# Optimization experiments

Hardware: AMD Instinct MI355X
Metric: run time of the kernel (lower is better)

Reference implementation:

```python
import jax, jax.numpy as jnp
from jax import lax
import numpy as np
import math

A = 9          # anchors per location
NC = 80        # classes
SCORE_T = 0.05
NMS_T = 0.5
DPI = 100      # detections_per_img (also per-level K in _inference)
BBOX_CLIP = math.log(1000.0 / 16.0)
LEVEL_SHAPES = [(64, 64), (32, 32), (16, 16), (8, 8)]
STRIDES = [8, 16, 32, 64]
BASE_SIZES = [32, 64, 128, 256]


def _conv(x, w, b):
    y = lax.conv_general_dilated(x, w, (1, 1), 'SAME', dimension_numbers=('NCHW', 'OIHW', 'NCHW'))
    return y + b[None, :, None, None]


def _head(feats, tower_w, tower_b, out_w, out_b, out_dim):
    outs = []
    for f in feats:
        x = f
        for i in range(tower_w.shape[0]):
            x = jax.nn.relu(_conv(x, tower_w[i], tower_b[i]))
        x = _conv(x, out_w, out_b)                     # [B, A*out_dim, H, W]
        B, _, H, W = x.shape
        x = x.reshape(B, A, out_dim, H, W).transpose(0, 3, 4, 1, 2).reshape(B, H * W * A, out_dim)
        outs.append(x)
    return outs


def _clip_boxes(b, img_h, img_w):
    x1 = jnp.clip(b[:, 0], 0.0, float(img_w)); y1 = jnp.clip(b[:, 1], 0.0, float(img_h))
    x2 = jnp.clip(b[:, 2], 0.0, float(img_w)); y2 = jnp.clip(b[:, 3], 0.0, float(img_h))
    return jnp.stack([x1, y1, x2, y2], axis=-1)


def _level_anchors(H, W, stride, s, img_h, img_w):
    # torchvision AnchorGenerator: sizes (s, s*2^(1/3), s*2^(2/3)), ratios (0.5,1,2)
    sizes = jnp.array([s, int(s * 2 ** (1 / 3)), int(s * 2 ** (2 / 3))], dtype=jnp.float32)
    ratios = jnp.array([0.5, 1.0, 2.0], dtype=jnp.float32)
    h_r = jnp.sqrt(ratios); w_r = 1.0 / h_r
    ws = (w_r[:, None] * sizes[None, :]).reshape(-1)
    hs = (h_r[:, None] * sizes[None, :]).reshape(-1)
    base = jnp.round(jnp.stack([-ws, -hs, ws, hs], axis=-1) / 2.0)   # [9,4]
    sx = (jnp.arange(W) * stride).astype(jnp.float32)
    sy = (jnp.arange(H) * stride).astype(jnp.float32)
    yy, xx = jnp.meshgrid(sy, sx, indexing='ij')
    shifts = jnp.stack([xx, yy, xx, yy], axis=-1).reshape(-1, 1, 4)   # [H*W,1,4]
    anch = (shifts + base[None]).reshape(-1, 4)                        # [H*W*A,4]
    return _clip_boxes(anch, img_h, img_w)


def _decode(rel, anch):
    # BoxCoder.decode_single with weights (1,1,1,1)
    w = anch[:, 2] - anch[:, 0]; h = anch[:, 3] - anch[:, 1]
    cx = anch[:, 0] + 0.5 * w;   cy = anch[:, 1] + 0.5 * h
    dx, dy = rel[:, 0], rel[:, 1]
    dw = jnp.minimum(rel[:, 2], BBOX_CLIP)
    dh = jnp.minimum(rel[:, 3], BBOX_CLIP)
    pcx = dx * w + cx; pcy = dy * h + cy
    pw = jnp.exp(dw) * w; ph = jnp.exp(dh) * h
    return jnp.stack([pcx - 0.5 * pw, pcy - 0.5 * ph, pcx + 0.5 * pw, pcy + 0.5 * ph], axis=-1)


def _pairwise_iou(boxes):
    area = (boxes[:, 2] - boxes[:, 0]) * (boxes[:, 3] - boxes[:, 1])
    lt = jnp.maximum(boxes[:, None, :2], boxes[None, :, :2])
    rb = jnp.minimum(boxes[:, None, 2:], boxes[None, :, 2:])
    wh = jnp.clip(rb - lt, 0.0)
    inter = wh[..., 0] * wh[..., 1]
    return inter / (area[:, None] + area[None, :] - inter + 1e-9)


def _per_image(logits, regs, anchors, img_h, img_w):
    bs, ss, ls = [], [], []
    for logit, reg, anch in zip(logits, regs, anchors):
        scores = jax.nn.sigmoid(logit).reshape(-1)                   # [N*NC]
        masked = jnp.where(scores > SCORE_T, scores, -1.0)
        top_s, idx = lax.top_k(masked, DPI)                          # fixed K = detections_per_img
        aidx = idx // NC
        lbl = idx % NC
        boxes = _clip_boxes(_decode(reg[aidx], anch[aidx]), img_h, img_w)
        valid = top_s > SCORE_T
        bs.append(boxes)
        ss.append(jnp.where(valid, top_s, -1.0))
        ls.append(jnp.where(valid, lbl, -1))
    boxes = jnp.concatenate(bs, 0); scores = jnp.concatenate(ss, 0); labels = jnp.concatenate(ls, 0)
    # batched (per-class) NMS via label coordinate offsets
    order = jnp.argsort(-scores)
    boxes_s = boxes[order]; scores_s = scores[order]; labels_s = labels[order]
    offset = labels_s.astype(boxes.dtype) * (float(max(img_h, img_w)) + 1.0)
    iou = lax.stop_gradient(_pairwise_iou(boxes_s + offset[:, None]))
    N = scores_s.shape[0]
    ar = jnp.arange(N)
    def body(i, keep):
        sup = keep[i] & (iou[i] > NMS_T) & (ar > i)
        return keep & ~sup
    keep = lax.fori_loop(0, N, body, scores_s > SCORE_T)
    fs, fi = lax.top_k(jnp.where(keep, scores_s, -1.0), DPI)
    ok = fs > SCORE_T
    fb = jnp.where(ok[:, None], boxes_s[fi], 0.0)
    fl = jnp.where(ok, labels_s[fi], -1)
    fs = jnp.where(ok, fs, 0.0)
    return fb, fs, fl


def setup_inputs() -> dict:
    key = jax.random.key(0)
    ks = jax.random.split(key, 8)
    B = 4
    w_scale = 0.04
    inp = {}
    shapes = [(B, 256, 64, 64), (B, 256, 32, 32), (B, 256, 16, 16), (B, 256, 8, 8)]
    for i, sh in enumerate(shapes):
        inp[f'f{i}'] = jax.random.normal(ks[i], sh, dtype=jnp.float32)
    inp['cls_tower_w'] = jax.random.normal(ks[4], (4, 256, 256, 3, 3), dtype=jnp.float32) * w_scale
    inp['cls_tower_b'] = jnp.zeros((4, 256), dtype=jnp.float32)
    inp['cls_out_w'] = jax.random.normal(ks[5], (A * NC, 256, 3, 3), dtype=jnp.float32) * w_scale
    inp['cls_out_b'] = jnp.full((A * NC,), -2.0, dtype=jnp.float32)  # prior-like bias
    inp['reg_tower_w'] = jax.random.normal(ks[6], (4, 256, 256, 3, 3), dtype=jnp.float32) * w_scale
    inp['reg_tower_b'] = jnp.zeros((4, 256), dtype=jnp.float32)
    inp['reg_out_w'] = jax.random.normal(ks[7], (A * 4, 256, 3, 3), dtype=jnp.float32) * w_scale
    inp['reg_out_b'] = jnp.zeros((A * 4,), dtype=jnp.float32)
    inp['image_h'] = 512
    inp['image_w'] = 512
    return inp


def reference(f0, f1, f2, f3, cls_tower_w, cls_tower_b, cls_out_w, cls_out_b,
              reg_tower_w, reg_tower_b, reg_out_w, reg_out_b, image_h, image_w):
    feats = [f0, f1, f2, f3]
    cls_logits = _head(feats, cls_tower_w, cls_tower_b, cls_out_w, cls_out_b, NC)   # list of [B,Ni,NC]
    bbox_regs = _head(feats, reg_tower_w, reg_tower_b, reg_out_w, reg_out_b, 4)     # list of [B,Ni,4]
    anchors = [_level_anchors(H, W, st, s, image_h, image_w)
               for (H, W), st, s in zip(LEVEL_SHAPES, STRIDES, BASE_SIZES)]
    fn = lambda ls, rs: _per_image(ls, rs, anchors, image_h, image_w)
    boxes, scores, labels = jax.vmap(fn)(tuple(cls_logits), tuple(bbox_regs))
    return boxes, scores, labels
```

## Files before the change

### kernel.cpp

```cpp
#include <hip/hip_runtime.h>
#include <math.h>

#define A_NUM 9
#define NCLS 80
#define IMG_KEY 3916800
#define IMG_REG 195840
#define CAP 8192
#define HBINS 16384

#define PCHUNK 12032
#define CHUNK_SLOTS 24064
#define CHUNK_BYTES (CHUNK_SLOTS * 16)
#define ACT_SLAB ((size_t)CHUNK_BYTES * 16)
#define WCHUNK_BYTES 40960
#define WCOG_BYTES (WCHUNK_BYTES * 16)

typedef _Float16 h8 __attribute__((ext_vector_type(8)));
typedef float fx4 __attribute__((ext_vector_type(4)));
typedef unsigned short u16;

__constant__ int   c_W[4]       = {64, 32, 16, 8};
__constant__ int   c_stride[4]  = {8, 16, 32, 64};
__constant__ float c_sizes[4][3]= {{32.f,40.f,50.f},{64.f,80.f,101.f},{128.f,161.f,203.f},{256.f,322.f,406.f}};
__constant__ int   c_keyOff[4]  = {0, 2949120, 3686400, 3870720};
__constant__ int   c_keyCnt[4]  = {2949120, 737280, 184320, 46080};
__constant__ int   c_regOff[4]  = {0, 147456, 184320, 193536};
__constant__ int   c_C[4]       = {66, 34, 18, 18};
__constant__ int   c_plvl[4]    = {0, 8712, 11024, 11672};
__constant__ int   c_pOff[4]    = {0, 1024, 1280, 1344};

__device__ __forceinline__ void gl_lds16(const void* g, void* l) {
    __builtin_amdgcn_global_load_lds(
        (const __attribute__((address_space(1))) void*)g,
        (__attribute__((address_space(3))) void*)l, 16, 0, 0);
}

__global__ __launch_bounds__(256) void pad16_k(
    const float* __restrict__ f0, const float* __restrict__ f1,
    const float* __restrict__ f2, const float* __restrict__ f3,
    char* __restrict__ Pin)
{
    int idx = blockIdx.x * 256 + threadIdx.x;
    const int PER_IMG = 16 * 2 * 1360;
    if (idx >= 4 * PER_IMG) return;
    int img = idx / PER_IMG;
    int r = idx - img * PER_IMG;
    int chunk = r / (2 * 1360);
    int r2 = r - chunk * (2 * 1360);
    int hfsel = r2 / 1360;
    int p = r2 - hfsel * 1360;
    int lvl = (p < 1024) ? 0 : (p < 1280 ? 1 : (p < 1344 ? 2 : 3));
    int u = p - c_pOff[lvl];
    int sh = 4 - lvl;
    int y = u >> sh;
    int xg = u & ((1 << sh) - 1);
    int x0 = xg * 4;
    int W = 64 >> lvl;
    const float* f = (lvl == 0) ? f0 : (lvl == 1) ? f1 : (lvl == 2) ? f2 : f3;
    int ci0 = chunk * 16 + hfsel * 8;
    float4 v[8];
    #pragma unroll
    for (int j = 0; j < 8; ++j)
        v[j] = *reinterpret_cast<const float4*>(
            f + ((size_t)(img * 256 + ci0 + j)) * (W * W) + y * W + x0);
    char* base = Pin + (size_t)img * ACT_SLAB + (size_t)chunk * CHUNK_BYTES;
    const int C = c_C[lvl];
    size_t rowSlot = (size_t)c_plvl[lvl] + (size_t)((y + 1) * 2 + hfsel) * C;
    #pragma unroll
    for (int c = 0; c < 4; ++c) {
        h8 hv, lv;
        #pragma unroll
        for (int j = 0; j < 8; ++j) {
            float val = (c == 0) ? v[j].x : (c == 1) ? v[j].y : (c == 2) ? v[j].z : v[j].w;
            _Float16 hh = (_Float16)val;
            hv[j] = hh;
            lv[j] = (_Float16)(val - (float)hh);
        }
        size_t slot = rowSlot + (x0 + c + 1);
        *reinterpret_cast<h8*>(base + slot * 16) = hv;
        *reinterpret_cast<h8*>(base + (slot + PCHUNK) * 16) = lv;
    }
}

__global__ __launch_bounds__(256) void repack16_k(
    const float* __restrict__ src, u16* __restrict__ dst,
    int C_out, int nCg, int total)
{
    int idx = blockIdx.x * 256 + threadIdx.x;
    if (idx >= total) return;
    int per = nCg * 16 * 1280;
    int layer = idx / per;
    int r = idx - layer * per;
    int cg = r / (16 * 1280);
    int r2 = r - cg * (16 * 1280);
    int chunk = r2 / 1280;
    int s = r2 - chunk * 1280;
    int co = s & 63;
    int r3 = s >> 6;
    int hfsel = r3 & 1;
    int kk = r3 >> 1;
    int coG = cg * 64 + co;
    float v[8];
    if (kk < 9 && coG < C_out) {
        const float* sp = src + ((size_t)(layer * C_out + coG)) * 2304
                        + (size_t)(chunk * 16 + hfsel * 8) * 9 + kk;
        #pragma unroll
        for (int j = 0; j < 8; ++j) v[j] = sp[j * 9];
    } else {
        #pragma unroll
        for (int j = 0; j < 8; ++j) v[j] = 0.f;
    }
    h8 hv, lv;
    #pragma unroll
    for (int j = 0; j < 8; ++j) {
        _Float16 hh = (_Float16)v[j];
        hv[j] = hh;
        lv[j] = (_Float16)(v[j] - (float)hh);
    }
    size_t e = ((size_t)((layer * nCg + cg) * 16 + chunk)) * 20480
             + (size_t)(kk >> 1) * 2048 + (size_t)(kk & 1) * 1024
             + (size_t)hfsel * 512 + (size_t)co * 8;
    *reinterpret_cast<h8*>(dst + e) = hv;
    *reinterpret_cast<h8*>(dst + e + 10240) = lv;
}

__global__ __launch_bounds__(256, 3) void conv16(
    const char* __restrict__ Pin, const char* __restrict__ bufIn, char* __restrict__ bufOut,
    const u16* __restrict__ repA, const float* __restrict__ bA,
    const u16* __restrict__ repB, const float* __restrict__ bB,
    unsigned* __restrict__ keys, float* __restrict__ regb,
    int mode, int usePin)
{
    const int tid = threadIdx.x;
    const int lane = tid & 63;
    const int wv = tid >> 6;

    int img, head, coBase, C_out, epi, tile;
    if (mode == 0) {
        int hw = blockIdx.x;
        int logical = (hw & 7) * 88 + (hw >> 3);
        int z = logical / 88;
        int rem = logical - z * 88;
        tile = rem >> 2;
        coBase = (rem & 3) * 64;
        img = z & 3; head = z >> 2;
        C_out = 256; epi = 0;
    } else {
        int hw = blockIdx.x;
        int logical = (hw & 7) * 143 + (hw >> 3);
        img = logical / 286;
        int rem = logical - img * 286;
        tile = rem / 13;
        int yy = rem - tile * 13;
        if (yy < 12) { head = 0; coBase = yy * 64; C_out = 720; epi = 1; }
        else         { head = 1; coBase = 0;       C_out = 36;  epi = 2; }
    }
    const float* bsel = head ? bB : bA;
    const u16* wsel = head ? repB : repA;
    const char* wBase = (const char*)wsel + (size_t)(coBase >> 6) * WCOG_BYTES;

    int lvl, ty, tx;
    if (tile < 16)      { lvl = 0; ty = tile >> 2; tx = tile & 3; }
    else if (tile < 20) { int u = tile - 16; lvl = 1; ty = u >> 1; tx = u & 1; }
    else if (tile == 20){ lvl = 2; ty = 0; tx = 0; }
    else                { lvl = 3; ty = 0; tx = 0; }
    const int W = 64 >> lvl;
    const int C = c_C[lvl];
    const int plvl = c_plvl[lvl];
    const int tileY = ty * 16, tileX = tx * 16;

    const char* srcB = usePin ? Pin + (size_t)img * ACT_SLAB
                              : bufIn + (size_t)(head * 4 + img) * ACT_SLAB;

    __shared__ alignas(16) char sA[10368];
    __shared__ alignas(16) char sB[20480];

    const int laneCol = lane & 15;
    const int g = lane >> 4;
    const int halfS = g & 1;
    const int tapS = g >> 1;
    const int laneBv = tapS * 2048 + halfS * 1024 + laneCol * 16;
    int laneAhi[5];
    int AloOff[5];
    #pragma unroll
    for (int k = 0; k < 5; ++k) {
        int kk = 2 * k + tapS; if (kk > 8) kk = 8;
        int ky = kk / 3;
        int kx = kk - ky * 3;
        laneAhi[k] = ky * 576 + halfS * 288 + (laneCol + kx) * 16;
        AloOff[k] = PCHUNK * 16
                  + (plvl + ((tileY + wv * 4 + ky) * 2 + halfS) * C
                     + tileX + laneCol + kx) * 16;
    }
    const int mtStride = 2 * C * 16;

    int aByte[3]; bool aOk[3];
    #pragma unroll
    for (int p = 0; p < 3; ++p) {
        int s = tid + 256 * p;
        aOk[p] = (s < 648);
        int sc = aOk[p] ? s : 647;
        int row = sc / 36;
        int q = sc - row * 36;
        int hf = q / 18;
        int col = q - hf * 18;
        aByte[p] = (plvl + ((tileY + row) * 2 + hf) * C + tileX + col) * 16;
    }

    fx4 acc[4][4];
    #pragma unroll
    for (int mt = 0; mt < 4; ++mt)
        #pragma unroll
        for (int nt = 0; nt < 4; ++nt)
            acc[mt][nt] = (fx4){0.f, 0.f, 0.f, 0.f};

    #pragma unroll 1
    for (int ck = 0; ck < 16; ++ck) {
        const char* srcCk = srcB + (size_t)ck * CHUNK_BYTES;
        const char* wCk = wBase + (size_t)ck * WCHUNK_BYTES;
        const char* wLo = wCk + 20480;

        h8 Bl[2][4];
        #pragma unroll
        for (int nt = 0; nt < 4; ++nt)
            Bl[0][nt] = *reinterpret_cast<const h8*>(wLo + laneBv + nt * 256);

        #pragma unroll
        for (int p = 0; p < 3; ++p)
            if (aOk[p]) gl_lds16(srcCk + aByte[p], (char*)sA + (wv * 64 + 256 * p) * 16);
        for (int j = wv; j < 20; j += 4)
            gl_lds16(wCk + j * 1024 + lane * 16, (char*)sB + j * 1024);
        __syncthreads();

        #pragma unroll
        for (int k = 0; k < 5; ++k) {
            if (k < 4) {
                const char* wn = wLo + (k + 1) * 4096;
                #pragma unroll
                for (int nt = 0; nt < 4; ++nt)
                    Bl[(k + 1) & 1][nt] = *reinterpret_cast<const h8*>(wn + laneBv + nt * 256);
            }
            h8 Al[4];
            #pragma unroll
            for (int mt = 0; mt < 4; ++mt)
                Al[mt] = *reinterpret_cast<const h8*>(srcCk + AloOff[k] + mt * mtStride);
            const char* bk = sB + k * 4096;
            h8 Bh[4];
            #pragma unroll
            for (int nt = 0; nt < 4; ++nt)
                Bh[nt] = *reinterpret_cast<const h8*>(bk + laneBv + nt * 256);
            #pragma unroll
            for (int mt = 0; mt < 4; ++mt) {
                h8 Ah = *reinterpret_cast<const h8*>(sA + (wv * 4 + mt) * 576 + laneAhi[k]);
                #pragma unroll
                for (int nt = 0; nt < 4; ++nt) {
                    acc[mt][nt] = __builtin_amdgcn_mfma_f32_16x16x32_f16(Ah, Bh[nt], acc[mt][nt], 0, 0, 0);
                    acc[mt][nt] = __builtin_amdgcn_mfma_f32_16x16x32_f16(Ah, Bl[k & 1][nt], acc[mt][nt], 0, 0, 0);
                    acc[mt][nt] = __builtin_amdgcn_mfma_f32_16x16x32_f16(Al[mt], Bh[nt], acc[mt][nt], 0, 0, 0);
                }
            }
        }
        __syncthreads();
    }

    const int HW = W * W;
    if (epi == 0) {
        char* dstB = bufOut + (size_t)(head * 4 + img) * ACT_SLAB;
        _Float16* eW = reinterpret_cast<_Float16*>(sB + wv * 1024);
        const int ci8 = laneCol & 7;
        const int hf  = laneCol >> 3;
        const int rpx = lane & 15, rhalf = (lane >> 4) & 1, rplane = lane >> 5;
        const int rOff = rpx * 32 + rplane * 16 + rhalf * 8;
        const int rx = tileX + rpx;
        #pragma unroll
        for (int mt = 0; mt < 4; ++mt) {
            int y = tileY + wv * 4 + mt;
            bool yok = (y < W);
            #pragma unroll
            for (int nt = 0; nt < 4; ++nt) {
                int coG = coBase + nt * 16 + laneCol;
                float b = bsel[coG];
                #pragma unroll
                for (int i = 0; i < 4; ++i) {
                    float v = fmaxf(acc[mt][nt][i] + b, 0.f);
                    _Float16 hh = (_Float16)v;
                    _Float16 ll = (_Float16)(v - (float)hh);
                    int px = g * 4 + i;
                    eW[px * 32 + hf * 8 + ci8] = hh;
                    eW[px * 32 + 16 + hf * 8 + ci8] = ll;
                }
                __syncthreads();
                if (yok && rx < W) {
                    int chunkIdx = (coBase + nt * 16) >> 4;
                    size_t slot = (size_t)chunkIdx * CHUNK_SLOTS + (size_t)rplane * PCHUNK
                                + plvl + (size_t)((y + 1) * 2 + rhalf) * C + (rx + 1);
                    *reinterpret_cast<h8*>(dstB + slot * 16) =
                        *reinterpret_cast<const h8*>(eW + rOff);
                }
                __syncthreads();
            }
        }
    } else if (epi == 1) {
        unsigned* kb = keys + (size_t)img * IMG_KEY + c_keyOff[lvl];
        #pragma unroll
        for (int mt = 0; mt < 4; ++mt) {
            int y = tileY + wv * 4 + mt;
            int x0 = tileX + g * 4;
            if (y >= W || x0 >= W) continue;
            #pragma unroll
            for (int nt = 0; nt < 4; ++nt) {
                int coG = coBase + nt * 16 + laneCol;
                if (coG >= C_out) continue;
                float b = bsel[coG];
                unsigned kq[4];
                #pragma unroll
                for (int i = 0; i < 4; ++i) {
                    float sc = 1.0f / (1.0f + expf(-(acc[mt][nt][i] + b)));
                    kq[i] = (sc > 0.05f) ? __float_as_uint(sc) : 0u;
                }
                *reinterpret_cast<uint4*>(kb + (size_t)coG * HW + y * W + x0) =
                    make_uint4(kq[0], kq[1], kq[2], kq[3]);
            }
        }
    } else {
        float* rb = regb + (size_t)img * IMG_REG + c_regOff[lvl];
        #pragma unroll
        for (int mt = 0; mt < 4; ++mt) {
            int y = tileY + wv * 4 + mt;
            if (y >= W) continue;
            #pragma unroll
            for (int nt = 0; nt < 4; ++nt) {
                int coG = nt * 16 + laneCol;
                if (coG >= C_out) continue;
                float b = bsel[coG];
                int a = coG >> 2, jj = coG & 3;
                #pragma unroll
                for (int i = 0; i < 4; ++i) {
                    int x = tileX + g * 4 + i;
                    if (x >= W) continue;
                    rb[((size_t)(y * W + x) * A_NUM + a) * 4 + jj] = acc[mt][nt][i] + b;
                }
            }
        }
    }
}

__global__ __launch_bounds__(256) void hist_k(const unsigned* __restrict__ keys,
                                              unsigned* __restrict__ hist)
{
    int il = blockIdx.y, img = il >> 2, lvl = il & 3;
    int n = c_keyCnt[lvl];
    int chunk = blockIdx.x * 16384;
    if (chunk >= n) return;
    __shared__ unsigned h[HBINS];
    for (int t = threadIdx.x; t < HBINS; t += 256) h[t] = 0;
    __syncthreads();
    const uint4* k4 = (const uint4*)(keys + (size_t)img * IMG_KEY + c_keyOff[lvl]);
    int i0 = chunk >> 2, i1 = min(chunk + 16384, n) >> 2;
    for (int i = i0 + (int)threadIdx.x; i < i1; i += 256) {
        uint4 kv = k4[i];
        if (kv.x) atomicAdd(&h[kv.x >> 18], 1u);
        if (kv.y) atomicAdd(&h[kv.y >> 18], 1u);
        if (kv.z) atomicAdd(&h[kv.z >> 18], 1u);
        if (kv.w) atomicAdd(&h[kv.w >> 18], 1u);
    }
    __syncthreads();
    unsigned* gh = hist + (size_t)il * HBINS;
    for (int t = threadIdx.x; t < HBINS; t += 256)
        if (h[t]) atomicAdd(&gh[t], h[t]);
}

__global__ __launch_bounds__(256) void thresh_k(const unsigned* __restrict__ hist,
                                                unsigned* __restrict__ tbin)
{
    const unsigned* h = hist + (size_t)blockIdx.x * HBINS;
    __shared__ unsigned cs[256];
    int tid = threadIdx.x;
    unsigned s = 0;
    int base = tid * 64;
    for (int q = 0; q < 64; ++q) { int b = base + q; if (b >= 1) s += h[b]; }
    cs[tid] = s;
    __syncthreads();
    if (tid == 0) {
        unsigned total = 0, sel = 0;
        for (int c = 255; c >= 0; --c) {
            if (total + cs[c] >= 100u) {
                int lo = (c == 0) ? 1 : c * 64;
                for (int b = c * 64 + 63; b >= lo; --b) {
                    total += h[b];
                    if (total >= 100u) { sel = (unsigned)b; break; }
                }
                break;
            }
            total += cs[c];
        }
        tbin[blockIdx.x] = sel;
    }
}

__global__ __launch_bounds__(256) void compact_k(const unsigned* __restrict__ keys,
                                                 const unsigned* __restrict__ tbin,
                                                 unsigned* __restrict__ cnt,
                                                 uint2* __restrict__ comp)
{
    int il = blockIdx.y, img = il >> 2, lvl = il & 3;
    int n = c_keyCnt[lvl];
    int chunk = blockIdx.x * 16384;
    if (chunk >= n) return;
    const uint4* k4 = (const uint4*)(keys + (size_t)img * IMG_KEY + c_keyOff[lvl]);
    unsigned thr = tbin[il] << 18;
    int shift = 12 - 2 * lvl;
    int hwm = (1 << shift) - 1;
    int i0 = chunk >> 2, i1 = min(chunk + 16384, n) >> 2;
    __shared__ unsigned lcnt, lbase, lcur;
    if (threadIdx.x == 0) { lcnt = 0; lcur = 0; }
    __syncthreads();
    unsigned myc = 0;
    for (int i = i0 + (int)threadIdx.x; i < i1; i += 256) {
        uint4 kv = k4[i];
        myc += (kv.x != 0u && kv.x >= thr);
        myc += (kv.y != 0u && kv.y >= thr);
        myc += (kv.z != 0u && kv.z >= thr);
        myc += (kv.w != 0u && kv.w >= thr);
    }
    if (myc) atomicAdd(&lcnt, myc);
    __syncthreads();
    if (threadIdx.x == 0 && lcnt) lbase = atomicAdd(&cnt[il], lcnt);
    __syncthreads();
    if (lcnt == 0) return;
    uint2* c = comp + (size_t)il * CAP;
    for (int i = i0 + (int)threadIdx.x; i < i1; i += 256) {
        uint4 kv = k4[i];
        unsigned kk[4] = {kv.x, kv.y, kv.z, kv.w};
        #pragma unroll
        for (int j = 0; j < 4; ++j) {
            unsigned key = kk[j];
            if (key != 0u && key >= thr) {
                int t = i * 4 + j;
                int co = t >> shift, p = t & hwm;
                int a = co / NCLS, cls = co - a * NCLS;
                unsigned idx = (unsigned)((p * A_NUM + a) * NCLS + cls);
                unsigned pos = lbase + atomicAdd(&lcur, 1u);
                if (pos < CAP) c[pos] = make_uint2(key, idx);
            }
        }
    }
}

__global__ __launch_bounds__(256) void topsort_k(const unsigned* __restrict__ cnt,
                                                 const uint2* __restrict__ comp,
                                                 uint2* __restrict__ topk)
{
    __shared__ unsigned long long s[CAP];
    int il = blockIdx.x, tid = threadIdx.x;
    int n = (int)min(cnt[il], (unsigned)CAP);
    const uint2* c = comp + (size_t)il * CAP;
    for (int i = tid; i < CAP; i += 256) {
        unsigned long long v = 0ull;
        if (i < n) {
            uint2 e = c[i];
            v = ((unsigned long long)e.x << 32) | (unsigned long long)(~e.y);
        }
        s[i] = v;
    }
    for (int k = 2; k <= CAP; k <<= 1) {
        for (int j = k >> 1; j > 0; j >>= 1) {
            __syncthreads();
            for (int p = tid; p < CAP / 2; p += 256) {
                int i = ((p & ~(j - 1)) << 1) | (p & (j - 1));
                int ixj = i | j;
                unsigned long long a = s[i], b = s[ixj];
                if (((i & k) == 0) ? (a < b) : (a > b)) { s[i] = b; s[ixj] = a; }
            }
        }
    }
    __syncthreads();
    if (tid < 100) {
        unsigned long long v = s[tid];
        topk[il * 100 + tid] = make_uint2((unsigned)(v >> 32), ~(unsigned)(v & 0xFFFFFFFFull));
    }
}

__global__ void decode_k(const uint2* __restrict__ topk, const float* __restrict__ regb,
                         float* __restrict__ cboxes, float* __restrict__ cscores,
                         int* __restrict__ clabels, const int* __restrict__ ph, const int* __restrict__ pw)
{
    int il = blockIdx.x, img = il >> 2, lvl = il & 3;
    int j = threadIdx.x;
    if (j >= 100) return;
    float imgW = (float)pw[0], imgH = (float)ph[0];
    uint2 tk = topk[il * 100 + j];
    int outP = img * 400 + lvl * 100 + j;
    if (tk.x == 0u) {
        cboxes[outP * 4 + 0] = 0.f; cboxes[outP * 4 + 1] = 0.f;
        cboxes[outP * 4 + 2] = 0.f; cboxes[outP * 4 + 3] = 0.f;
        cscores[outP] = -1.0f; clabels[outP] = -1;
        return;
    }
    float score = __uint_as_float(tk.x);
    unsigned idx = tk.y;
    int aidx = (int)(idx / NCLS);
    int lbl  = (int)(idx - (unsigned)aidx * NCLS);
    int a = aidx % A_NUM, p = aidx / A_NUM;
    int W = c_W[lvl];
    int y = p / W, x = p - y * W;
    int r = a / 3, si = a - r * 3;
    float ratio = (r == 0) ? 0.5f : ((r == 1) ? 1.0f : 2.0f);
    float size = c_sizes[lvl][si];
    float hr = sqrtf(ratio);
    float wr = 1.0f / hr;
    float wsz = wr * size, hsz = hr * size;
    float bw = rintf(wsz * 0.5f), bh = rintf(hsz * 0.5f);
    float sx = (float)(x * c_stride[lvl]), sy = (float)(y * c_stride[lvl]);
    float ax1 = fminf(fmaxf(sx - bw, 0.f), imgW);
    float ay1 = fminf(fmaxf(sy - bh, 0.f), imgH);
    float ax2 = fminf(fmaxf(sx + bw, 0.f), imgW);
    float ay2 = fminf(fmaxf(sy + bh, 0.f), imgH);
    float aw = ax2 - ax1, ah = ay2 - ay1;
    float cx = ax1 + 0.5f * aw, cy = ay1 + 0.5f * ah;
    const float* rel = regb + (size_t)img * IMG_REG + c_regOff[lvl] + (size_t)aidx * 4;
    float dx = rel[0], dy = rel[1];
    float dw = fminf(rel[2], 4.135166556742356f);
    float dh = fminf(rel[3], 4.135166556742356f);
    float pcx = dx * aw + cx, pcy = dy * ah + cy;
    float pwd = expf(dw) * aw, phd = expf(dh) * ah;
    float x1 = pcx - 0.5f * pwd, y1 = pcy - 0.5f * phd;
    float x2 = pcx + 0.5f * pwd, y2 = pcy + 0.5f * phd;
    cboxes[outP * 4 + 0] = fminf(fmaxf(x1, 0.f), imgW);
    cboxes[outP * 4 + 1] = fminf(fmaxf(y1, 0.f), imgH);
    cboxes[outP * 4 + 2] = fminf(fmaxf(x2, 0.f), imgW);
    cboxes[outP * 4 + 3] = fminf(fmaxf(y2, 0.f), imgH);
    cscores[outP] = score;
    clabels[outP] = lbl;
}

__global__ __launch_bounds__(512) void nms_k(const float* __restrict__ cboxes,
                                             const float* __restrict__ cscores,
                                             const int* __restrict__ clabels,
                                             const int* __restrict__ ph, const int* __restrict__ pw,
                                             float* __restrict__ out)
{
    int img = blockIdx.x, tid = threadIdx.x;
    __shared__ float sSc[512];
    __shared__ int   sPos[512];
    __shared__ float bx1[400], by1[400], bx2[400], by2[400], sAr[400];
    __shared__ int   sKeep[400], sLbl[400];
    float imgH = (float)ph[0], imgW = (float)pw[0];
    float offm = fmaxf(imgH, imgW) + 1.0f;

    sSc[tid] = (tid < 400) ? cscores[img * 400 + tid] : -3.0f;
    sPos[tid] = tid;
    __syncthreads();

    for (int k = 2; k <= 512; k <<= 1) {
        for (int jj = k >> 1; jj > 0; jj >>= 1) {
            int ixj = tid ^ jj;
            if (ixj > tid) {
                float s1 = sSc[tid], s2 = sSc[ixj];
                int p1 = sPos[tid], p2 = sPos[ixj];
                bool bef = (s1 > s2) || (s1 == s2 && p1 < p2);
                bool sw = ((tid & k) == 0) ? (!bef) : bef;
                if (sw) { sSc[tid] = s2; sSc[ixj] = s1; sPos[tid] = p2; sPos[ixj] = p1; }
            }
            __syncthreads();
        }
    }

    if (tid < 400) {
        int p = sPos[tid];
        int lbl = clabels[img * 400 + p];
        float ofs = (float)lbl * offm;
        float x1 = cboxes[(img * 400 + p) * 4 + 0] + ofs;
        float y1 = cboxes[(img * 400 + p) * 4 + 1] + ofs;
        float x2 = cboxes[(img * 400 + p) * 4 + 2] + ofs;
        float y2 = cboxes[(img * 400 + p) * 4 + 3] + ofs;
        bx1[tid] = x1; by1[tid] = y1; bx2[tid] = x2; by2[tid] = y2;
        sAr[tid] = (x2 - x1) * (y2 - y1);
        sLbl[tid] = lbl;
        sKeep[tid] = (sSc[tid] > 0.05f) ? 1 : 0;
    }
    __syncthreads();

    for (int i = 0; i < 400; ++i) {
        if (sKeep[i]) {
            for (int j2 = i + 1 + tid; j2 < 400; j2 += 512) {
                float ltx = fmaxf(bx1[i], bx1[j2]), lty = fmaxf(by1[i], by1[j2]);
                float rbx = fminf(bx2[i], bx2[j2]), rby = fminf(by2[i], by2[j2]);
                float ww = fmaxf(rbx - ltx, 0.f), hh = fmaxf(rby - lty, 0.f);
                float inter = ww * hh;
                float iou = inter / (((sAr[i] + sAr[j2]) - inter) + 1e-9f);
                if (iou > 0.5f) sKeep[j2] = 0;
            }
        }
        __syncthreads();
    }

    if (tid == 0) {
        int rank = 0;
        for (int i = 0; i < 400 && rank < 100; ++i) {
            if (sKeep[i]) {
                int p = sPos[i];
                for (int kk = 0; kk < 4; ++kk)
                    out[(img * 100 + rank) * 4 + kk] = cboxes[(img * 400 + p) * 4 + kk];
                out[1600 + img * 100 + rank] = sSc[i];
                out[2000 + img * 100 + rank] = (float)sLbl[i];
                ++rank;
            }
        }
        for (; rank < 100; ++rank) {
            for (int kk = 0; kk < 4; ++kk) out[(img * 100 + rank) * 4 + kk] = 0.f;
            out[1600 + img * 100 + rank] = 0.f;
            out[2000 + img * 100 + rank] = -1.0f;
        }
    }
}

extern "C" void kernel_launch(void* const* d_in, const int* in_sizes, int n_in,
                              void* d_out, int out_size, void* d_ws, size_t ws_size,
                              hipStream_t stream)
{
    const float* f0 = (const float*)d_in[0];
    const float* f1 = (const float*)d_in[1];
    const float* f2 = (const float*)d_in[2];
    const float* f3 = (const float*)d_in[3];
    const float* cls_tw = (const float*)d_in[4];
    const float* cls_tb = (const float*)d_in[5];
    const float* cls_ow = (const float*)d_in[6];
    const float* cls_ob = (const float*)d_in[7];
    const float* reg_tw = (const float*)d_in[8];
    const float* reg_tb = (const float*)d_in[9];
    const float* reg_ow = (const float*)d_in[10];
    const float* reg_ob = (const float*)d_in[11];
    const int* ph = (const int*)d_in[12];
    const int* pw = (const int*)d_in[13];
    float* out = (float*)d_out;

    char* ws = (char*)d_ws;
    size_t off = 0;
    auto alloc = [&](size_t bytes) -> void* {
        void* p = ws + off;
        off = (off + bytes + 1023) & ~(size_t)1023;
        return p;
    };
    const size_t KEYS = (size_t)4 * IMG_KEY * 4;
    const size_t ACT8 = ACT_SLAB * 8;
    char*     Pin    = (char*)alloc(ACT_SLAB * 4 + 32768);
    char*     slabA  = (char*)alloc((KEYS > ACT8 ? KEYS : ACT8) + 32768);
    unsigned* keys   = (unsigned*)slabA;
    char*     actA   = slabA;
    char*     actB   = (char*)alloc(ACT8 + 32768);
    u16*      repCT  = (u16*)alloc((size_t)16 * WCOG_BYTES);
    u16*      repRT  = (u16*)alloc((size_t)16 * WCOG_BYTES);
    u16*      repCO  = (u16*)alloc((size_t)12 * WCOG_BYTES);
    u16*      repRO  = (u16*)alloc((size_t)1 * WCOG_BYTES);
    float*    regb   = (float*)alloc((size_t)4 * IMG_REG * 4);
    unsigned* hist   = (unsigned*)alloc((size_t)16 * HBINS * 4);
    unsigned* cnt    = (unsigned*)alloc(16 * 4);
    unsigned* tbin   = (unsigned*)alloc(16 * 4);
    uint2*    comp   = (uint2*)alloc((size_t)16 * CAP * 8);
    uint2*    topk   = (uint2*)alloc((size_t)1600 * 8);
    float*    cboxes = (float*)alloc((size_t)4 * 400 * 4 * 4);
    float*    cscores= (float*)alloc((size_t)4 * 400 * 4);
    int*      clabels= (int*)alloc((size_t)4 * 400 * 4);

    hipMemsetAsync(Pin, 0, ACT_SLAB * 4, stream);
    hipMemsetAsync(actA, 0, ACT8, stream);
    hipMemsetAsync(actB, 0, ACT8, stream);
    hipMemsetAsync(hist, 0, (size_t)16 * HBINS * 4, stream);
    hipMemsetAsync(cnt, 0, 64, stream);

    {
        int tPad = 4 * 16 * 2 * 1360;
        pad16_k<<<(tPad + 255) / 256, 256, 0, stream>>>(f0, f1, f2, f3, Pin);
        int tT = 4 * 4 * 16 * 1280;
        repack16_k<<<(tT + 255) / 256, 256, 0, stream>>>(cls_tw, repCT, 256, 4, tT);
        repack16_k<<<(tT + 255) / 256, 256, 0, stream>>>(reg_tw, repRT, 256, 4, tT);
        int tCO = 12 * 16 * 1280;
        repack16_k<<<(tCO + 255) / 256, 256, 0, stream>>>(cls_ow, repCO, 720, 12, tCO);
        int tRO = 16 * 1280;
        repack16_k<<<(tRO + 255) / 256, 256, 0, stream>>>(reg_ow, repRO, 36, 1, tRO);
    }

    const size_t RL = (size_t)4 * 16 * 20480;
    conv16<<<704, 256, 0, stream>>>(Pin, Pin, actA,
        repCT, cls_tb, repRT, reg_tb, keys, regb, 0, 1);
    conv16<<<704, 256, 0, stream>>>(Pin, actA, actB,
        repCT + RL, cls_tb + 256, repRT + RL, reg_tb + 256, keys, regb, 0, 0);
    conv16<<<704, 256, 0, stream>>>(Pin, actB, actA,
        repCT + 2 * RL, cls_tb + 512, repRT + 2 * RL, reg_tb + 512, keys, regb, 0, 0);
    conv16<<<704, 256, 0, stream>>>(Pin, actA, actB,
        repCT + 3 * RL, cls_tb + 768, repRT + 3 * RL, reg_tb + 768, keys, regb, 0, 0);
    conv16<<<1144, 256, 0, stream>>>(Pin, actB, nullptr,
        repCO, cls_ob, repRO, reg_ob, keys, regb, 1, 0);

    hist_k<<<dim3(180, 16), 256, 0, stream>>>(keys, hist);
    thresh_k<<<16, 256, 0, stream>>>(hist, tbin);
    compact_k<<<dim3(180, 16), 256, 0, stream>>>(keys, tbin, cnt, comp);
    topsort_k<<<16, 256, 0, stream>>>(cnt, comp, topk);
    decode_k<<<16, 128, 0, stream>>>(topk, regb, cboxes, cscores, clabels, ph, pw);
    nms_k<<<4, 512, 0, stream>>>(cboxes, cscores, clabels, ph, pw, out);
}
```

Baseline: 1.316 ms.

## Double-buffer LDS tiles in conv16 to prefetch the next channel chunk during MFMA

```diff
diff --git a/kernel.cpp b/kernel.cpp
--- a/kernel.cpp
+++ b/kernel.cpp
@@ -124,7 +124,7 @@
     *reinterpret_cast<h8*>(dst + e + 10240) = lv;
 }
 
-__global__ __launch_bounds__(256, 3) void conv16(
+__global__ __launch_bounds__(256, 2) void conv16(
     const char* __restrict__ Pin, const char* __restrict__ bufIn, char* __restrict__ bufOut,
     const u16* __restrict__ repA, const float* __restrict__ bA,
     const u16* __restrict__ repB, const float* __restrict__ bB,
@@ -172,8 +172,8 @@
     const char* srcB = usePin ? Pin + (size_t)img * ACT_SLAB
                               : bufIn + (size_t)(head * 4 + img) * ACT_SLAB;
 
-    __shared__ alignas(16) char sA[10368];
-    __shared__ alignas(16) char sB[20480];
+    __shared__ alignas(16) char sA[2][10368];
+    __shared__ alignas(16) char sB[2][20480];
 
     const int laneCol = lane & 15;
     const int g = lane >> 4;
@@ -214,59 +214,80 @@
         for (int nt = 0; nt < 4; ++nt)
             acc[mt][nt] = (fx4){0.f, 0.f, 0.f, 0.f};
 
+    {
+        const char* srcCk = srcB;
+        const char* wCk = wBase;
+        #pragma unroll
+        for (int p = 0; p < 3; ++p)
+            if (aOk[p]) gl_lds16(srcCk + aByte[p], (char*)sA[0] + (wv * 64 + 256 * p) * 16);
+        for (int j = wv; j < 20; j += 4)
+            gl_lds16(wCk + j * 1024 + lane * 16, (char*)sB[0] + j * 1024);
+    }
+    asm volatile("s_waitcnt vmcnt(0)" ::: "memory");
+    __builtin_amdgcn_s_barrier();
+
     #pragma unroll 1
     for (int ck = 0; ck < 16; ++ck) {
+        const int cur = ck & 1;
         const char* srcCk = srcB + (size_t)ck * CHUNK_BYTES;
-        const char* wCk = wBase + (size_t)ck * WCHUNK_BYTES;
-        const char* wLo = wCk + 20480;
-
-        h8 Bl[2][4];
+        const char* wLo = wBase + (size_t)ck * WCHUNK_BYTES + 20480;
+
+        h8 Bl[2][4], Al[2][4];
         #pragma unroll
         for (int nt = 0; nt < 4; ++nt)
             Bl[0][nt] = *reinterpret_cast<const h8*>(wLo + laneBv + nt * 256);
-
-        #pragma unroll
-        for (int p = 0; p < 3; ++p)
-            if (aOk[p]) gl_lds16(srcCk + aByte[p], (char*)sA + (wv * 64 + 256 * p) * 16);
-        for (int j = wv; j < 20; j += 4)
-            gl_lds16(wCk + j * 1024 + lane * 16, (char*)sB + j * 1024);
-        __syncthreads();
+        #pragma unroll
+        for (int mt = 0; mt < 4; ++mt)
+            Al[0][mt] = *reinterpret_cast<const h8*>(srcCk + AloOff[0] + mt * mtStride);
+
+        if (ck < 15) {
+            const char* srcN = srcB + (size_t)(ck + 1) * CHUNK_BYTES;
+            const char* wN = wBase + (size_t)(ck + 1) * WCHUNK_BYTES;
+            #pragma unroll
+            for (int p = 0; p < 3; ++p)
+                if (aOk[p]) gl_lds16(srcN + aByte[p], (char*)sA[cur ^ 1] + (wv * 64 + 256 * p) * 16);
+            for (int j = wv; j < 20; j += 4)
+                gl_lds16(wN + j * 1024 + lane * 16, (char*)sB[cur ^ 1] + j * 1024);
+        }
 
         #pragma unroll
         for (int k = 0; k < 5; ++k) {
+            const int sl = k & 1;
             if (k < 4) {
-                const char* wn = wLo + (k + 1) * 4096;
+                const char* wlk = wLo + (k + 1) * 4096;
                 #pragma unroll
                 for (int nt = 0; nt < 4; ++nt)
-                    Bl[(k + 1) & 1][nt] = *reinterpret_cast<const h8*>(wn + laneBv + nt * 256);
-            }
-            h8 Al[4];
-            #pragma unroll
-            for (int mt = 0; mt < 4; ++mt)
-                Al[mt] = *reinterpret_cast<const h8*>(srcCk + AloOff[k] + mt * mtStride);
-            const char* bk = sB + k * 4096;
+                    Bl[sl ^ 1][nt] = *reinterpret_cast<const h8*>(wlk + laneBv + nt * 256);
+                #pragma unroll
+                for (int mt = 0; mt < 4; ++mt)
+                    Al[sl ^ 1][mt] = *reinterpret_cast<const h8*>(srcCk + AloOff[k + 1] + mt * mtStride);
+            }
+            const char* bk = sB[cur] + k * 4096;
             h8 Bh[4];
             #pragma unroll
             for (int nt = 0; nt < 4; ++nt)
                 Bh[nt] = *reinterpret_cast<const h8*>(bk + laneBv + nt * 256);
             #pragma unroll
             for (int mt = 0; mt < 4; ++mt) {
-                h8 Ah = *reinterpret_cast<const h8*>(sA + (wv * 4 + mt) * 576 + laneAhi[k]);
+                h8 Ah = *reinterpret_cast<const h8*>(sA[cur] + (wv * 4 + mt) * 576 + laneAhi[k]);
                 #pragma unroll
                 for (int nt = 0; nt < 4; ++nt) {
                     acc[mt][nt] = __builtin_amdgcn_mfma_f32_16x16x32_f16(Ah, Bh[nt], acc[mt][nt], 0, 0, 0);
-                    acc[mt][nt] = __builtin_amdgcn_mfma_f32_16x16x32_f16(Ah, Bl[k & 1][nt], acc[mt][nt], 0, 0, 0);
-                    acc[mt][nt] = __builtin_amdgcn_mfma_f32_16x16x32_f16(Al[mt], Bh[nt], acc[mt][nt], 0, 0, 0);
+                    acc[mt][nt] = __builtin_amdgcn_mfma_f32_16x16x32_f16(Ah, Bl[sl][nt], acc[mt][nt], 0, 0, 0);
+                    acc[mt][nt] = __builtin_amdgcn_mfma_f32_16x16x32_f16(Al[sl][mt], Bh[nt], acc[mt][nt], 0, 0, 0);
                 }
             }
         }
-        __syncthreads();
+
+        asm volatile("s_waitcnt vmcnt(0)" ::: "memory");
+        __builtin_amdgcn_sched_barrier(0);
+        __builtin_amdgcn_s_barrier();
     }
 
     const int HW = W * W;
     if (epi == 0) {
         char* dstB = bufOut + (size_t)(head * 4 + img) * ACT_SLAB;
-        _Float16* eW = reinterpret_cast<_Float16*>(sB + wv * 1024);
+        _Float16* eW = reinterpret_cast<_Float16*>((char*)sB[0] + wv * 1024);
         const int ci8 = laneCol & 7;
         const int hf  = laneCol >> 3;
         const int rpx = lane & 15, rhalf = (lane >> 4) & 1, rplane = lane >> 5;
```

Result: slower. 1.398 ms (+6.2%).
